# Kernel optimization log

Hardware: AMD Instinct MI355X
Metric: run time of the kernel (lower is better)

The kernel has to match this reference:

```python
import jax, jax.numpy as jnp
import numpy as np

B, C, H, W = 16, 64, 64, 64
HD = 128


def skew(x):
    # x: [B,C,H,W] -> [B,C,H,H+W-1], row r shifted right by r
    b, c, h, w = x.shape
    sw = h + w - 1
    xp = jnp.pad(x, ((0, 0), (0, 0), (0, 0), (0, h - 1)))
    cols = (jnp.arange(sw)[None, :] - jnp.arange(h)[:, None]) % sw  # [H,SW]
    return xp[:, :, jnp.arange(h)[:, None], cols]


def unskew(x):
    # x: [B,C,H,SW] -> [B,C,H,W]
    b, c, h, sw = x.shape
    w = sw - h + 1
    cols = jnp.arange(w)[None, :] + jnp.arange(h)[:, None]  # [H,W]
    return x[:, :, jnp.arange(h)[:, None], cols]


def setup_inputs() -> dict:
    key = jax.random.key(0)
    k1, k2, k3, k4, k5 = jax.random.split(key, 5)
    s_is = 1.0 / np.sqrt(C)
    s_ss = 1.0 / np.sqrt(HD * 2)
    return {
        "x": jax.random.normal(k1, (B, C, H, W), jnp.float32),
        "w_is": jax.random.uniform(k2, (5 * HD, C), jnp.float32, -s_is, s_is),   # 1x1 conv (mask B, k=1 => plain)
        "b_is": jax.random.uniform(k3, (5 * HD,), jnp.float32, -s_is, s_is),
        "w_ss": jax.random.uniform(k4, (5 * HD, HD, 2), jnp.float32, -s_ss, s_ss),  # Conv1d k=2
        "b_ss": jax.random.uniform(k5, (5 * HD,), jnp.float32, -s_ss, s_ss),
    }


def reference(x, w_is, b_is, w_ss, b_ss):
    hd = w_ss.shape[1]
    sk = skew(x)  # [B,C,H,SW]
    # input-to-state: 1x1 conv over skewed map
    i_s = jnp.einsum("oc,bchw->bohw", w_is, sk) + b_is[None, :, None, None]
    is_cols = jnp.moveaxis(i_s, -1, 0)  # [SW,B,5hd,H]
    w0, w1 = w_ss[:, :, 0], w_ss[:, :, 1]  # taps for h[t-1], h[t]
    bsz, h_dim = x.shape[0], x.shape[2]

    def step(carry, ic):
        h_prev, c_prev = carry
        h_sh = jnp.pad(h_prev, ((0, 0), (0, 0), (1, 0)))[:, :, :-1]
        s_s = (jnp.einsum("oi,bih->boh", w1, h_prev)
               + jnp.einsum("oi,bih->boh", w0, h_sh)
               + b_ss[None, :, None])
        gates = ic + s_s
        o, fl, fu, i, g = jnp.split(gates, 5, axis=1)
        o, fl, fu, i = map(jax.nn.sigmoid, (o, fl, fu, i))
        g = jnp.tanh(g)
        c_sh = jnp.pad(c_prev, ((0, 0), (0, 0), (1, 0)))[:, :, :-1]
        c = fl * c_prev + fu * c_sh + i * g
        h = o * jnp.tanh(c)
        return (h, c), h

    z = jnp.zeros((bsz, hd, h_dim), x.dtype)
    _, hs = jax.lax.scan(step, (z, z), is_cols)
    hs = jnp.moveaxis(hs, 0, -1)  # [B,hd,H,SW]
    return unskew(hs)
```

## Files before the change

kernel.cpp:

```cpp
#include <hip/hip_runtime.h>

typedef __attribute__((ext_vector_type(8))) short bf16x8;
typedef __attribute__((ext_vector_type(4))) float f32x4;
typedef __attribute__((ext_vector_type(4))) uint  u32x4;
typedef __attribute__((ext_vector_type(2))) uint  u32x2;

#define B_   16
#define C_   64
#define H_   64
#define W_   64
#define HD_  128
#define K_   320
#define SW_  127

#define NG    4
#define GH    32
#define NCG   64
#define TC    16
#define NT    704
#define ROWS  160
#define NKT   10
#define GPS   17

#define HSLOT  131072LL
#define CBX    524288LL
#define CNT    557056LL
#define GCNT   559104LL
#define AFB    561152LL
#define AF_N   204800LL
#define XT     765952LL
#define XT_N   4194304LL
#define WS_MIN (AFB + AF_N)
#define WS_XT  (XT + XT_N)

#define POLL_CAP (1 << 20)

__device__ __forceinline__ float sigm(float v) { return 1.f / (1.f + __expf(-v)); }
__device__ __forceinline__ float tanh_fast(float v) {
    float e = __expf(2.f * v);
    return 1.f - 2.f / (e + 1.f);
}

__device__ __forceinline__ int rload(int* p) {
    return __hip_atomic_load(p, __ATOMIC_RELAXED, __HIP_MEMORY_SCOPE_AGENT);
}
__device__ __forceinline__ void rbump(int* p) {
    __hip_atomic_fetch_add(p, 1, __ATOMIC_RELAXED, __HIP_MEMORY_SCOPE_AGENT);
}
__device__ __forceinline__ void wait_ge(int* p, int tgt) {
    int guard = 0;
    while (rload(p) < tgt) { if (++guard > POLL_CAP) break; }
    __atomic_signal_fence(__ATOMIC_ACQUIRE);
}

__device__ __forceinline__ void stu_nw(uint* p, uint v) {
    asm volatile("global_store_dword %0, %1, off sc0 sc1" :: "v"(p), "v"(v) : "memory");
}
__device__ __forceinline__ void st2_nw(uint* p, u32x2 v) {
    asm volatile("global_store_dwordx2 %0, %1, off sc0 sc1" :: "v"(p), "v"(v) : "memory");
}

__device__ __forceinline__ void poll1(const uint* p, uint want, u32x4& A) {
    int guard = 0;
    while (true) {
        u32x4 a;
        asm volatile("global_load_dwordx4 %0, %1, off sc0 sc1\n\ts_waitcnt vmcnt(0)"
                     : "=&v"(a) : "v"(p) : "memory");
        uint m = a[0] & a[1] & a[2] & a[3];
        uint o = a[0] | a[1] | a[2] | a[3];
        bool ok = want ? ((m & 1u) != 0u) : ((o & 1u) == 0u);
        if (ok || ++guard > POLL_CAP) { A = a; return; }
    }
}

__device__ __forceinline__ uint bf16hi(uint u) { return (u + 0x7FFFu + ((u >> 16) & 1u)) >> 16; }
__device__ __forceinline__ uint2 splitbf(float v) {
    uint uh = bf16hi(__float_as_uint(v));
    float rl = v - __uint_as_float(uh << 16);
    uint ul = bf16hi(__float_as_uint(rl));
    return make_uint2(uh, ul);
}

__global__ void lstm_prep(const float* __restrict__ w_is,
                          const float* __restrict__ w_ss,
                          float* __restrict__ ws, long long n_ws)
{
    const long long stride = (long long)gridDim.x * blockDim.x;
    const long long t0 = (long long)blockIdx.x * blockDim.x + threadIdx.x;
    uint* wsu = (uint*)ws;

    for (long long i = t0; i < 524288LL + 32768LL; i += stride) {
        long long a = (i < 524288LL) ? i : (CBX + (i - 524288LL));
        stu_nw(wsu + a, 0x00000001u);
    }
    for (long long i = CNT + t0; i < CNT + 4096; i += stride)
        stu_nw(wsu + i, 0u);

    if (n_ws >= WS_MIN) {
        ushort* af = (ushort*)(ws + AFB);
        for (long long e = t0; e < AF_N; e += stride) {
            int idx   = (int)e;
            int chunk = idx >> 9;
            int lane  = (idx >> 3) & 63;
            int jj    = idx & 7;
            int g  = chunk / (10 * NKT);
            int rm = chunk % (10 * NKT);
            int rt = rm / NKT, kt = rm % NKT;
            int m = lane & 15, quad = lane >> 4;
            int r = rt * 16 + m;
            int q = r >> 5, hl = r & 31;
            int o = q * HD_ + g * GH + hl;
            int k = kt * 32 + quad * 8 + jj;
            float v;
            if (k < C_)            v = w_is[o * C_ + k];
            else if (k < C_ + HD_) v = w_ss[(o * HD_ + (k - C_)) * 2 + 1];
            else                   v = w_ss[(o * HD_ + (k - C_ - HD_)) * 2 + 0];
            uint uh = bf16hi(__float_as_uint(v));
            float rl = v - __uint_as_float(uh << 16);
            uint ul = bf16hi(__float_as_uint(rl));
            int base = chunk * 1024 + lane * 16 + jj;
            af[base]     = (ushort)uh;
            af[base + 8] = (ushort)ul;
        }
    }
}

__global__ void lstm_xpose(const float* __restrict__ x, float* __restrict__ ws)
{
    __shared__ float L[64 * 65];
    const int b = blockIdx.x >> 6, hr = blockIdx.x & 63;
    const int tid = threadIdx.x;
    #pragma unroll
    for (int it = 0; it < 16; ++it) {
        int c = it * 4 + (tid >> 6), w = tid & 63;
        L[c * 65 + w] = x[(((size_t)b * C_ + c) * H_ + hr) * W_ + w];
    }
    __syncthreads();
    float* xt = ws + XT;
    #pragma unroll
    for (int it = 0; it < 16; ++it) {
        int w = it * 4 + (tid >> 6), c = tid & 63;
        xt[(((size_t)b * H_ + hr) * W_ + w) * C_ + c] = L[c * 65 + w];
    }
}

__global__ void __launch_bounds__(NT, 2) lstm_persist(
    const float* __restrict__ x,
    const float* __restrict__ ws_c,
    const float* __restrict__ b_is,
    const float* __restrict__ b_ss,
    float* __restrict__ out,
    float* __restrict__ ws,
    int use_xt)
{
    __shared__ uint  Bf[NKT * 576];
    __shared__ float Gp[ROWS * GPS];
    __shared__ float Cs[2][17 * GH];
    __shared__ float bias_s[ROWS];

    const int tid = threadIdx.x;
    const int cgp = blockIdx.x >> 2;
    const int g   = blockIdx.x & 3;
    const int n0  = cgp * TC;
    const int inb  = (n0 & 63) != 0;
    const int hasr = ((n0 + TC) & 63) != 0;

    uint* hring = (uint*)ws;
    uint* cring = (uint*)(ws + CBX);
    int*  gcntp = (int*)(ws + GCNT);
    const float* xt = ws_c + XT;
    const uint4* afq = (const uint4*)(ws_c + AFB);

    if (tid < ROWS) {
        int q = tid >> 5, hl = tid & 31;
        int o = q * HD_ + g * GH + hl;
        bias_s[tid] = b_is[o] + b_ss[o];
    }
    if (tid < 17 * GH) Cs[0][tid] = 0.f;
    if (tid >= 544 && tid < 544 + GH) Cs[1][tid - 544] = 0.f;

    const int lane = tid & 63;
    const int wv   = tid >> 6;
    const int quad = lane >> 4;
    const int colc = lane & 15;
    uint* bfr = &Bf[lane * 8 + ((lane >> 2) << 2)];

    const int cp  = tid >> 5;
    const int ch  = tid & 31;
    const int pq  = (ch >> 1) & 3;
    const int pj0 = (ch & 1) * 4;
    const int kta = 2 + (ch >> 3);
    const int laneA = pq * 16 + ((cp >= 1) ? (cp - 1) : 0);
    const int laneB = pq * 16 + ((cp <= 15) ? cp : 0);
    uint* bfA = &Bf[laneA * 8 + ((laneA >> 2) << 2) + kta * 576 + (pj0 >> 1)];
    uint* bfB = &Bf[laneB * 8 + ((laneB >> 2) << 2) + (kta + 4) * 576 + (pj0 >> 1)];
    const uint* hbase = hring + (size_t)(n0 - 1 + cp) * 128 + ch * 4;
    const int pskip = (cp == 0 && !inb);

    const int xi = tid - 544;
    const int xkt = xi >> 6, xl = xi & 63;
    const int xq = xl >> 4, xcolc = xl & 15;
    const int xc0 = xkt * 32 + xq * 8;
    const int xn = n0 + xcolc, xb = xn >> 6, xhr = xn & 63;
    uint* bfX = &Bf[xl * 8 + ((xl >> 2) << 2) + xkt * 576];

    const int ci = tid - 672;

    bf16x8 Ahr[NKT], Alr[NKT];
    if (wv < 10) {
        const uint4* ap0 = afq + (size_t)((g * 10 + wv) * NKT) * 128 + lane * 2;
        #pragma unroll
        for (int kt = 0; kt < NKT; ++kt) {
            uint4 ha = ap0[kt * 128];
            Ahr[kt] = *(bf16x8*)&ha;
            asm volatile("" : "+v"(Ahr[kt]));
            uint4 la = ap0[kt * 128 + 1];
            Alr[kt] = *(bf16x8*)&la;
            asm volatile("" : "+v"(Alr[kt]));
        }
    }

    __syncthreads();

    for (int j = 0; j < SW_; ++j) {
        const uint want = ((j - 1) >> 2) & 1u;
        const uint wtag = (j >> 2) & 1u;

        if (tid < 544) {
            u32x4 a = {0, 0, 0, 0};
            if (j > 0 && !pskip)
                poll1(hbase + (size_t)((j - 1) & 3) * HSLOT, want, a);
            uint2 e0 = splitbf(__uint_as_float(a[0]));
            uint2 e1 = splitbf(__uint_as_float(a[1]));
            uint2 e2 = splitbf(__uint_as_float(a[2]));
            uint2 e3 = splitbf(__uint_as_float(a[3]));
            u32x2 hp = {e0.x | (e1.x << 16), e2.x | (e3.x << 16)};
            u32x2 lp = {e0.y | (e1.y << 16), e2.y | (e3.y << 16)};
            if (cp >= 1)  { *(u32x2*)bfA = hp; *(u32x2*)(bfA + 4) = lp; }
            if (cp <= 15) { *(u32x2*)bfB = hp; *(u32x2*)(bfB + 4) = lp; }
        } else if (tid < 672) {
            float xv[8];
            int w = j - xhr;
            if ((unsigned)w < (unsigned)W_) {
                if (use_xt) {
                    const float* xp = xt + (((size_t)xb * H_ + xhr) * W_ + w) * C_ + xc0;
                    f32x4 va = *(const f32x4*)xp, vb = *(const f32x4*)(xp + 4);
                    #pragma unroll
                    for (int r = 0; r < 4; ++r) { xv[r] = va[r]; xv[4 + r] = vb[r]; }
                } else {
                    #pragma unroll
                    for (int r = 0; r < 8; ++r)
                        xv[r] = x[(((size_t)xb * C_ + xc0 + r) * H_ + xhr) * W_ + w];
                }
            } else {
                #pragma unroll
                for (int r = 0; r < 8; ++r) xv[r] = 0.f;
            }
            uint hw[4], lw[4];
            #pragma unroll
            for (int p = 0; p < 4; ++p) {
                uint2 e0 = splitbf(xv[2 * p]), e1 = splitbf(xv[2 * p + 1]);
                hw[p] = e0.x | (e1.x << 16);
                lw[p] = e0.y | (e1.y << 16);
            }
            *(uint4*)bfX       = make_uint4(hw[0], hw[1], hw[2], hw[3]);
            *(uint4*)(bfX + 4) = make_uint4(lw[0], lw[1], lw[2], lw[3]);
        } else if (ci >= 0 && ci < 8) {
            if (inb && j > 0) {
                u32x4 cv;
                const uint* cpx = cring +
                    (((size_t)((j - 1) & 3) * NCG + (cgp - 1)) * NG + g) * GH + ci * 4;
                poll1(cpx, want, cv);
                #pragma unroll
                for (int r = 0; r < 4; ++r)
                    Cs[j & 1][ci * 4 + r] = __uint_as_float(cv[r]);
            }
        } else if (ci == 8) {
            if (j >= 4 && hasr) wait_ge(gcntp + (cgp + 1) * 32, 4 * (j - 2));
        }
        __syncthreads();
        if (tid == 0) rbump(gcntp + cgp * 32);

        if (wv < 10) {
            f32x4 acc0 = {0.f, 0.f, 0.f, 0.f};
            f32x4 acc1 = {0.f, 0.f, 0.f, 0.f};
            __builtin_amdgcn_s_setprio(1);
            #pragma unroll
            for (int kt = 0; kt < NKT; kt += 2) {
                const uint* bp0 = bfr + kt * 576;
                uint4 hb0 = *(const uint4*)bp0;
                uint4 lb0 = *(const uint4*)(bp0 + 4);
                const uint* bp1 = bfr + (kt + 1) * 576;
                uint4 hb1 = *(const uint4*)bp1;
                uint4 lb1 = *(const uint4*)(bp1 + 4);
                bf16x8 Bh0 = *(bf16x8*)&hb0, Bl0 = *(bf16x8*)&lb0;
                bf16x8 Bh1 = *(bf16x8*)&hb1, Bl1 = *(bf16x8*)&lb1;
                acc0 = __builtin_amdgcn_mfma_f32_16x16x32_bf16(Ahr[kt],     Bh0, acc0, 0, 0, 0);
                acc1 = __builtin_amdgcn_mfma_f32_16x16x32_bf16(Ahr[kt + 1], Bh1, acc1, 0, 0, 0);
                acc0 = __builtin_amdgcn_mfma_f32_16x16x32_bf16(Ahr[kt],     Bl0, acc0, 0, 0, 0);
                acc1 = __builtin_amdgcn_mfma_f32_16x16x32_bf16(Ahr[kt + 1], Bl1, acc1, 0, 0, 0);
                acc0 = __builtin_amdgcn_mfma_f32_16x16x32_bf16(Alr[kt],     Bh0, acc0, 0, 0, 0);
                acc1 = __builtin_amdgcn_mfma_f32_16x16x32_bf16(Alr[kt + 1], Bh1, acc1, 0, 0, 0);
                acc0 = __builtin_amdgcn_mfma_f32_16x16x32_bf16(Alr[kt],     Bl0, acc0, 0, 0, 0);
                acc1 = __builtin_amdgcn_mfma_f32_16x16x32_bf16(Alr[kt + 1], Bl1, acc1, 0, 0, 0);
            }
            __builtin_amdgcn_s_setprio(0);
            #pragma unroll
            for (int r = 0; r < 4; ++r)
                Gp[(wv * 16 + quad * 4 + r) * GPS + colc] = acc0[r] + acc1[r];
        }
        __syncthreads();

        if (tid < GH * TC) {
            const int hl = tid & 31, col = tid >> 5;
            int n = n0 + col, b = n >> 6, hr = n & 63;
            float go  = Gp[(0 * GH + hl) * GPS + col] + bias_s[0 * GH + hl];
            float gfl = Gp[(1 * GH + hl) * GPS + col] + bias_s[1 * GH + hl];
            float gfu = Gp[(2 * GH + hl) * GPS + col] + bias_s[2 * GH + hl];
            float gi  = Gp[(3 * GH + hl) * GPS + col] + bias_s[3 * GH + hl];
            float gg  = Gp[(4 * GH + hl) * GPS + col] + bias_s[4 * GH + hl];
            float so = sigm(go), sfl = sigm(gfl), sfu = sigm(gfu), si = sigm(gi);
            float tg = tanh_fast(gg);
            float cp_ = Cs[j & 1][(col + 1) * GH + hl];
            float cs = Cs[j & 1][col * GH + hl];
            float cv = sfl * cp_ + sfu * cs + si * tg;
            float hv = so * tanh_fast(cv);
            Cs[(j + 1) & 1][(col + 1) * GH + hl] = cv;

            uint pk = (__float_as_uint(hv) & ~1u) | wtag;
            uint other = (uint)__shfl_xor((int)pk, 1);
            if (!(hl & 1)) {
                u32x2 pv = {pk, other};
                st2_nw(hring + (size_t)(j & 3) * HSLOT + (size_t)n * 128 + g * GH + (hl & ~1), pv);
            }
            if (col == TC - 1) {
                uint cpk = (__float_as_uint(cv) & ~1u) | wtag;
                stu_nw(cring + (((size_t)(j & 3) * NCG + cgp) * NG + g) * GH + hl, cpk);
            }
            int w = j - hr;
            if ((unsigned)w < (unsigned)W_)
                out[(((size_t)b * HD_ + g * GH + hl) * H_ + hr) * W_ + w] = hv;
        }
    }
}

extern "C" void kernel_launch(void* const* d_in, const int* in_sizes, int n_in,
                              void* d_out, int out_size, void* d_ws, size_t ws_size,
                              hipStream_t stream)
{
    const float* x    = (const float*)d_in[0];
    const float* w_is = (const float*)d_in[1];
    const float* b_is = (const float*)d_in[2];
    const float* w_ss = (const float*)d_in[3];
    const float* b_ss = (const float*)d_in[4];
    float* out = (float*)d_out;
    float* ws  = (float*)d_ws;

    const long long n_ws = (long long)(ws_size / 4);
    const int use_xt = (n_ws >= WS_XT) ? 1 : 0;

    hipLaunchKernelGGL(lstm_prep, dim3(1024), dim3(256), 0, stream,
                       w_is, w_ss, ws, n_ws);
    if (use_xt)
        hipLaunchKernelGGL(lstm_xpose, dim3(B_ * H_), dim3(256), 0, stream, x, ws);

    hipLaunchKernelGGL(lstm_persist, dim3(NG * NCG), dim3(NT), 0, stream,
                       x, ws, b_is, b_ss, out, ws, use_xt);
}
```

Before: 496.1 us.

## Overlap next-step h/x fragment staging with gate math in persistent LSTM

Restructures the per-column loop so the x-fragment build and the neighbor h/c polling for step j+1 are done by dedicated waves (8-11) while waves 0-7 compute the gate nonlinearities for step j. This removes one barrier-separated phase per step. h polling is consolidated into fewer threads issuing eight wide loads each. The block grows to 768 threads with a launch-bounds hint of 3 blocks, and the MFMA chain is split into four independent accumulators. The changes risk register pressure and longer poll latency per thread in exchange for fewer serialized phases.

```diff
diff --git a/kernel.cpp b/kernel.cpp
--- a/kernel.cpp
+++ b/kernel.cpp
@@ -17,7 +17,7 @@
 #define GH    32
 #define NCG   64
 #define TC    16
-#define NT    704
+#define NT    768
 #define ROWS  160
 #define NKT   10
 #define GPS   17
@@ -71,6 +71,33 @@
         bool ok = want ? ((m & 1u) != 0u) : ((o & 1u) == 0u);
         if (ok || ++guard > POLL_CAP) { A = a; return; }
     }
+}
+
+__device__ __forceinline__ bool try8(const uint* p, uint want,
+                                     u32x4& a0, u32x4& a1, u32x4& a2, u32x4& a3,
+                                     u32x4& a4, u32x4& a5, u32x4& a6, u32x4& a7) {
+    asm volatile(
+        "global_load_dwordx4 %0, %8, off sc0 sc1\n\t"
+        "global_load_dwordx4 %1, %8, off offset:16 sc0 sc1\n\t"
+        "global_load_dwordx4 %2, %8, off offset:128 sc0 sc1\n\t"
+        "global_load_dwordx4 %3, %8, off offset:144 sc0 sc1\n\t"
+        "global_load_dwordx4 %4, %8, off offset:256 sc0 sc1\n\t"
+        "global_load_dwordx4 %5, %8, off offset:272 sc0 sc1\n\t"
+        "global_load_dwordx4 %6, %8, off offset:384 sc0 sc1\n\t"
+        "global_load_dwordx4 %7, %8, off offset:400 sc0 sc1\n\t"
+        "s_waitcnt vmcnt(0)"
+        : "=&v"(a0), "=&v"(a1), "=&v"(a2), "=&v"(a3),
+          "=&v"(a4), "=&v"(a5), "=&v"(a6), "=&v"(a7)
+        : "v"(p) : "memory");
+    uint m = a0[0] & a0[1] & a0[2] & a0[3] & a1[0] & a1[1] & a1[2] & a1[3]
+           & a2[0] & a2[1] & a2[2] & a2[3] & a3[0] & a3[1] & a3[2] & a3[3]
+           & a4[0] & a4[1] & a4[2] & a4[3] & a5[0] & a5[1] & a5[2] & a5[3]
+           & a6[0] & a6[1] & a6[2] & a6[3] & a7[0] & a7[1] & a7[2] & a7[3];
+    uint o = a0[0] | a0[1] | a0[2] | a0[3] | a1[0] | a1[1] | a1[2] | a1[3]
+           | a2[0] | a2[1] | a2[2] | a2[3] | a3[0] | a3[1] | a3[2] | a3[3]
+           | a4[0] | a4[1] | a4[2] | a4[3] | a5[0] | a5[1] | a5[2] | a5[3]
+           | a6[0] | a6[1] | a6[2] | a6[3] | a7[0] | a7[1] | a7[2] | a7[3];
+    return want ? ((m & 1u) != 0u) : ((o & 1u) == 0u);
 }
 
 __device__ __forceinline__ uint bf16hi(uint u) { return (u + 0x7FFFu + ((u >> 16) & 1u)) >> 16; }
@@ -144,7 +171,7 @@
     }
 }
 
-__global__ void __launch_bounds__(NT, 2) lstm_persist(
+__global__ void __launch_bounds__(NT, 3) lstm_persist(
     const float* __restrict__ x,
     const float* __restrict__ ws_c,
     const float* __restrict__ b_is,
@@ -185,26 +212,30 @@
     const int colc = lane & 15;
     uint* bfr = &Bf[lane * 8 + ((lane >> 2) << 2)];
 
-    const int cp  = tid >> 5;
-    const int ch  = tid & 31;
-    const int pq  = (ch >> 1) & 3;
-    const int pj0 = (ch & 1) * 4;
-    const int kta = 2 + (ch >> 3);
-    const int laneA = pq * 16 + ((cp >= 1) ? (cp - 1) : 0);
-    const int laneB = pq * 16 + ((cp <= 15) ? cp : 0);
-    uint* bfA = &Bf[laneA * 8 + ((laneA >> 2) << 2) + kta * 576 + (pj0 >> 1)];
-    uint* bfB = &Bf[laneB * 8 + ((laneB >> 2) << 2) + (kta + 4) * 576 + (pj0 >> 1)];
-    const uint* hbase = hring + (size_t)(n0 - 1 + cp) * 128 + ch * 4;
-    const int pskip = (cp == 0 && !inb);
-
-    const int xi = tid - 544;
-    const int xkt = xi >> 6, xl = xi & 63;
+    const int xi = tid - 512;
+    const int xkt = (xi >> 6) & 1, xl = xi & 63;
     const int xq = xl >> 4, xcolc = xl & 15;
     const int xc0 = xkt * 32 + xq * 8;
     const int xn = n0 + xcolc, xb = xn >> 6, xhr = xn & 63;
     uint* bfX = &Bf[xl * 8 + ((xl >> 2) << 2) + xkt * 576];
 
-    const int ci = tid - 672;
+    const int pl    = tid - 640;
+    const int col16 = (pl >> 2) & 15;
+    const int sub   = pl & 3;
+    const int laneT = sub * 16 + col16;
+    const int laneS = sub * 16 + col16 + 1;
+    uint* pA = &Bf[laneT * 8 + ((laneT >> 2) << 2)];
+    uint* pB = &Bf[laneS * 8 + ((laneS >> 2) << 2)];
+    const uint* hb10 = hring + (size_t)(n0 + col16) * 128 + sub * 8;
+
+    const int ql = tid - 704;
+    const int bkt  = 6 + ((ql >> 3) & 3);
+    const int bquad = (ql >> 1) & 3;
+    const int bj0h = (ql & 1) * 2;
+    const int laneB0 = bquad * 16;
+    uint* pC = &Bf[laneB0 * 8 + ((laneB0 >> 2) << 2) + bkt * 576 + bj0h];
+    const uint* hb11 = hring + (size_t)(n0 - 1) * 128 + (ql & 31) * 4;
+    const int ci = ql - 32;
 
     bf16x8 Ahr[NKT], Alr[NKT];
     if (wv < 10) {
@@ -220,96 +251,99 @@
         }
     }
 
-    __syncthreads();
+#define XBUILD(JJ)                                                              \
+    {                                                                           \
+        float xv[8];                                                            \
+        int w = (JJ) - xhr;                                                     \
+        if ((unsigned)w < (unsigned)W_) {                                       \
+            if (use_xt) {                                                       \
+                const float* xp = xt + (((size_t)xb * H_ + xhr) * W_ + w) * C_ + xc0; \
+                f32x4 va = *(const f32x4*)xp, vb = *(const f32x4*)(xp + 4);     \
+                _Pragma("unroll")                                               \
+                for (int r = 0; r < 4; ++r) { xv[r] = va[r]; xv[4 + r] = vb[r]; } \
+            } else {                                                            \
+                _Pragma("unroll")                                               \
+                for (int r = 0; r < 8; ++r)                                     \
+                    xv[r] = x[(((size_t)xb * C_ + xc0 + r) * H_ + xhr) * W_ + w]; \
+            }                                                                   \
+        } else {                                                                \
+            _Pragma("unroll")                                                   \
+            for (int r = 0; r < 8; ++r) xv[r] = 0.f;                            \
+        }                                                                       \
+        uint hw[4], lw[4];                                                      \
+        _Pragma("unroll")                                                       \
+        for (int p = 0; p < 4; ++p) {                                           \
+            uint2 e0 = splitbf(xv[2 * p]), e1 = splitbf(xv[2 * p + 1]);         \
+            hw[p] = e0.x | (e1.x << 16);                                        \
+            lw[p] = e0.y | (e1.y << 16);                                        \
+        }                                                                       \
+        *(uint4*)bfX       = make_uint4(hw[0], hw[1], hw[2], hw[3]);            \
+        *(uint4*)(bfX + 4) = make_uint4(lw[0], lw[1], lw[2], lw[3]);            \
+    }
+
+#define FRAG(MM, CA, CB)                                                        \
+    {                                                                           \
+        uint2 e0 = splitbf(__uint_as_float(CA[0])), e1 = splitbf(__uint_as_float(CA[1])); \
+        uint2 e2 = splitbf(__uint_as_float(CA[2])), e3 = splitbf(__uint_as_float(CA[3])); \
+        uint2 f0 = splitbf(__uint_as_float(CB[0])), f1 = splitbf(__uint_as_float(CB[1])); \
+        uint2 f2 = splitbf(__uint_as_float(CB[2])), f3 = splitbf(__uint_as_float(CB[3])); \
+        uint4 hi4 = make_uint4(e0.x | (e1.x << 16), e2.x | (e3.x << 16),        \
+                               f0.x | (f1.x << 16), f2.x | (f3.x << 16));       \
+        uint4 lo4 = make_uint4(e0.y | (e1.y << 16), e2.y | (e3.y << 16),        \
+                               f0.y | (f1.y << 16), f2.y | (f3.y << 16));       \
+        *(uint4*)(pA + (2 + (MM)) * 576)     = hi4;                             \
+        *(uint4*)(pA + (2 + (MM)) * 576 + 4) = lo4;                             \
+        if (col16 <= 14) {                                                      \
+            *(uint4*)(pB + (6 + (MM)) * 576)     = hi4;                         \
+            *(uint4*)(pB + (6 + (MM)) * 576 + 4) = lo4;                         \
+        }                                                                       \
+    }
+
+    if (wv == 8 || wv == 9) {
+        XBUILD(0)
+    } else if (wv == 10) {
+        uint4 z = make_uint4(0, 0, 0, 0);
+        #pragma unroll
+        for (int m = 0; m < 4; ++m) {
+            *(uint4*)(pA + (2 + m) * 576) = z;  *(uint4*)(pA + (2 + m) * 576 + 4) = z;
+            if (col16 <= 14) {
+                *(uint4*)(pB + (6 + m) * 576) = z;  *(uint4*)(pB + (6 + m) * 576 + 4) = z;
+            }
+        }
+    } else if (wv == 11 && ql < 32) {
+        u32x2 z2 = {0, 0};
+        *(u32x2*)pC = z2;  *(u32x2*)(pC + 4) = z2;
+    }
 
     for (int j = 0; j < SW_; ++j) {
-        const uint want = ((j - 1) >> 2) & 1u;
-        const uint wtag = (j >> 2) & 1u;
-
-        if (tid < 544) {
-            u32x4 a = {0, 0, 0, 0};
-            if (j > 0 && !pskip)
-                poll1(hbase + (size_t)((j - 1) & 3) * HSLOT, want, a);
-            uint2 e0 = splitbf(__uint_as_float(a[0]));
-            uint2 e1 = splitbf(__uint_as_float(a[1]));
-            uint2 e2 = splitbf(__uint_as_float(a[2]));
-            uint2 e3 = splitbf(__uint_as_float(a[3]));
-            u32x2 hp = {e0.x | (e1.x << 16), e2.x | (e3.x << 16)};
-            u32x2 lp = {e0.y | (e1.y << 16), e2.y | (e3.y << 16)};
-            if (cp >= 1)  { *(u32x2*)bfA = hp; *(u32x2*)(bfA + 4) = lp; }
-            if (cp <= 15) { *(u32x2*)bfB = hp; *(u32x2*)(bfB + 4) = lp; }
-        } else if (tid < 672) {
-            float xv[8];
-            int w = j - xhr;
-            if ((unsigned)w < (unsigned)W_) {
-                if (use_xt) {
-                    const float* xp = xt + (((size_t)xb * H_ + xhr) * W_ + w) * C_ + xc0;
-                    f32x4 va = *(const f32x4*)xp, vb = *(const f32x4*)(xp + 4);
-                    #pragma unroll
-                    for (int r = 0; r < 4; ++r) { xv[r] = va[r]; xv[4 + r] = vb[r]; }
-                } else {
-                    #pragma unroll
-                    for (int r = 0; r < 8; ++r)
-                        xv[r] = x[(((size_t)xb * C_ + xc0 + r) * H_ + xhr) * W_ + w];
-                }
-            } else {
-                #pragma unroll
-                for (int r = 0; r < 8; ++r) xv[r] = 0.f;
-            }
-            uint hw[4], lw[4];
-            #pragma unroll
-            for (int p = 0; p < 4; ++p) {
-                uint2 e0 = splitbf(xv[2 * p]), e1 = splitbf(xv[2 * p + 1]);
-                hw[p] = e0.x | (e1.x << 16);
-                lw[p] = e0.y | (e1.y << 16);
-            }
-            *(uint4*)bfX       = make_uint4(hw[0], hw[1], hw[2], hw[3]);
-            *(uint4*)(bfX + 4) = make_uint4(lw[0], lw[1], lw[2], lw[3]);
-        } else if (ci >= 0 && ci < 8) {
-            if (inb && j > 0) {
-                u32x4 cv;
-                const uint* cpx = cring +
-                    (((size_t)((j - 1) & 3) * NCG + (cgp - 1)) * NG + g) * GH + ci * 4;
-                poll1(cpx, want, cv);
-                #pragma unroll
-                for (int r = 0; r < 4; ++r)
-                    Cs[j & 1][ci * 4 + r] = __uint_as_float(cv[r]);
-            }
-        } else if (ci == 8) {
-            if (j >= 4 && hasr) wait_ge(gcntp + (cgp + 1) * 32, 4 * (j - 2));
-        }
         __syncthreads();
         if (tid == 0) rbump(gcntp + cgp * 32);
 
         if (wv < 10) {
-            f32x4 acc0 = {0.f, 0.f, 0.f, 0.f};
-            f32x4 acc1 = {0.f, 0.f, 0.f, 0.f};
+            f32x4 aA = {0.f, 0.f, 0.f, 0.f};
+            f32x4 aB = {0.f, 0.f, 0.f, 0.f};
+            f32x4 aC = {0.f, 0.f, 0.f, 0.f};
+            f32x4 aD = {0.f, 0.f, 0.f, 0.f};
             __builtin_amdgcn_s_setprio(1);
             #pragma unroll
-            for (int kt = 0; kt < NKT; kt += 2) {
-                const uint* bp0 = bfr + kt * 576;
-                uint4 hb0 = *(const uint4*)bp0;
-                uint4 lb0 = *(const uint4*)(bp0 + 4);
-                const uint* bp1 = bfr + (kt + 1) * 576;
-                uint4 hb1 = *(const uint4*)bp1;
-                uint4 lb1 = *(const uint4*)(bp1 + 4);
-                bf16x8 Bh0 = *(bf16x8*)&hb0, Bl0 = *(bf16x8*)&lb0;
-                bf16x8 Bh1 = *(bf16x8*)&hb1, Bl1 = *(bf16x8*)&lb1;
-                acc0 = __builtin_amdgcn_mfma_f32_16x16x32_bf16(Ahr[kt],     Bh0, acc0, 0, 0, 0);
-                acc1 = __builtin_amdgcn_mfma_f32_16x16x32_bf16(Ahr[kt + 1], Bh1, acc1, 0, 0, 0);
-                acc0 = __builtin_amdgcn_mfma_f32_16x16x32_bf16(Ahr[kt],     Bl0, acc0, 0, 0, 0);
-                acc1 = __builtin_amdgcn_mfma_f32_16x16x32_bf16(Ahr[kt + 1], Bl1, acc1, 0, 0, 0);
-                acc0 = __builtin_amdgcn_mfma_f32_16x16x32_bf16(Alr[kt],     Bh0, acc0, 0, 0, 0);
-                acc1 = __builtin_amdgcn_mfma_f32_16x16x32_bf16(Alr[kt + 1], Bh1, acc1, 0, 0, 0);
-                acc0 = __builtin_amdgcn_mfma_f32_16x16x32_bf16(Alr[kt],     Bl0, acc0, 0, 0, 0);
-                acc1 = __builtin_amdgcn_mfma_f32_16x16x32_bf16(Alr[kt + 1], Bl1, acc1, 0, 0, 0);
+            for (int kt = 0; kt < NKT; ++kt) {
+                const uint* bp = bfr + kt * 576;
+                uint4 hb = *(const uint4*)bp;
+                uint4 lb = *(const uint4*)(bp + 4);
+                bf16x8 Bh = *(bf16x8*)&hb, Bl = *(bf16x8*)&lb;
+                aA = __builtin_amdgcn_mfma_f32_16x16x32_bf16(Ahr[kt], Bh, aA, 0, 0, 0);
+                aB = __builtin_amdgcn_mfma_f32_16x16x32_bf16(Ahr[kt], Bl, aB, 0, 0, 0);
+                aC = __builtin_amdgcn_mfma_f32_16x16x32_bf16(Alr[kt], Bh, aC, 0, 0, 0);
+                aD = __builtin_amdgcn_mfma_f32_16x16x32_bf16(Alr[kt], Bl, aD, 0, 0, 0);
             }
             __builtin_amdgcn_s_setprio(0);
             #pragma unroll
             for (int r = 0; r < 4; ++r)
-                Gp[(wv * 16 + quad * 4 + r) * GPS + colc] = acc0[r] + acc1[r];
+                Gp[(wv * 16 + quad * 4 + r) * GPS + colc] = (aA[r] + aB[r]) + (aC[r] + aD[r]);
         }
         __syncthreads();
+
+        const uint wtag = (j >> 2) & 1u;
 
         if (tid < GH * TC) {
             const int hl = tid & 31, col = tid >> 5;
@@ -340,8 +374,52 @@
             int w = j - hr;
             if ((unsigned)w < (unsigned)W_)
                 out[(((size_t)b * HD_ + g * GH + hl) * H_ + hr) * W_ + w] = hv;
+        } else if (wv == 8 || wv == 9) {
+            if (j + 1 < SW_) { XBUILD(j + 1) }
+        } else if (wv == 10) {
+            if (j + 1 < SW_) {
+                const uint* p = hb10 + (size_t)(j & 3) * HSLOT;
+                u32x4 a0, a1, a2, a3, a4, a5, a6, a7;
+                int guard = 0;
+                while (!try8(p, wtag, a0, a1, a2, a3, a4, a5, a6, a7)) {
+                    if (++guard > POLL_CAP) break;
+                }
+                FRAG(0, a0, a1)
+                FRAG(1, a2, a3)
+                FRAG(2, a4, a5)
+                FRAG(3, a6, a7)
+            }
+        } else {
+            if (ql < 32) {
+                if (j + 1 < SW_ && inb) {
+                    u32x4 a;
+                    poll1(hb11 + (size_t)(j & 3) * HSLOT, wtag, a);
+                    uint2 e0 = splitbf(__uint_as_float(a[0]));
+                    uint2 e1 = splitbf(__uint_as_float(a[1]));
+                    uint2 e2 = splitbf(__uint_as_float(a[2]));
+                    uint2 e3 = splitbf(__uint_as_float(a[3]));
+                    u32x2 hp = {e0.x | (e1.x << 16), e2.x | (e3.x << 16)};
+                    u32x2 lp = {e0.y | (e1.y << 16), e2.y | (e3.y << 16)};
+                    *(u32x2*)pC = hp;  *(u32x2*)(pC + 4) = lp;
+                }
+            } else if (ci >= 0 && ci < 8) {
+                if (j + 1 < SW_ && inb) {
+                    u32x4 cv4;
+                    const uint* cpx = cring +
+                        (((size_t)(j & 3) * NCG + (cgp - 1)) * NG + g) * GH + ci * 4;
+                    poll1(cpx, wtag, cv4);
+                    #pragma unroll
+                    for (int r = 0; r < 4; ++r)
+                        Cs[(j + 1) & 1][ci * 4 + r] = __uint_as_float(cv4[r]);
+                }
+            } else if (ci == 8) {
+                if (j >= 3 && j + 1 < SW_ && hasr)
+                    wait_ge(gcntp + (cgp + 1) * 32, 4 * (j - 1));
+            }
         }
     }
+#undef XBUILD
+#undef FRAG
 }
 
 extern "C" void kernel_launch(void* const* d_in, const int* in_sizes, int n_in,
```

After: 633.2 us. +27.6%, slower.
